# Kernel optimization log

Hardware: AMD Instinct MI355X
Metric: run time of the kernel (lower is better)

## Reference

```python
import jax, jax.numpy as jnp
import numpy as np

S, B, H, K, P = 512, 64, 8, 12, 9        # seq_len, input_bits, num_heads, bits_per_neuron, position bits
L = 2 * B + P                            # head input bits = 137
T = 2 ** K                               # RAM table entries per neuron = 4096
THRESH = H // 2                          # majority-vote threshold


def setup_inputs() -> dict:
    key = jax.random.key(0)
    k1, k2, k3 = jax.random.split(key, 3)
    tokens = jax.random.randint(k1, (S, B), 0, 2, dtype=jnp.int32)           # bit tokens
    conn = jax.random.randint(k2, (H, B, K), 0, L, dtype=jnp.int32)          # random neuron connections
    ram = jnp.round(jax.random.uniform(k3, (H, B, T), dtype=jnp.float32))    # binary RAM contents
    return {"tokens": tokens, "conn": conn, "ram": ram}


def _partial_addr(bits, idx, mask, w):
    # bits: [M, nbits] int; idx/mask: [H,B,K]; w: [K]. Returns [H,B,M] partial RAM address.
    g = bits[:, idx]                                           # [M,H,B,K]
    contrib = jnp.sum(g * (mask.astype(jnp.int32) * w), axis=-1)  # [M,H,B]
    return jnp.moveaxis(contrib, 0, -1)                        # [H,B,M]


def reference(tokens, conn, ram):
    w = (2 ** jnp.arange(K)).astype(jnp.int32)                 # bit weight per connection slot
    # Each connection reads from concat(query_bits[B], key_bits[B], rel_pos_bits[P]).
    is_q = conn < B
    is_k = (conn >= B) & (conn < 2 * B)
    is_r = conn >= 2 * B
    qi = jnp.where(is_q, conn, 0)
    ki = jnp.where(is_k, conn - B, 0)
    ri = jnp.where(is_r, conn - 2 * B, 0)
    d = jnp.arange(S)
    relbits = ((d[:, None] >> jnp.arange(P)) & 1).astype(jnp.int32)  # [S,P] binary rel distance
    # RAM address decomposes additively over the three bit sources.
    Aq = _partial_addr(tokens, qi, is_q, w)                    # [H,B,S] query part (per i)
    Ak = _partial_addr(tokens, ki, is_k, w)                    # [H,B,S] key part (per j)
    Ar = _partial_addr(relbits, ri, is_r, w)                   # [H,B,S] rel-dist part (per i-j)
    dij = jnp.maximum(d[:, None] - d[None, :], 0)              # [S,S] causal rel distance
    addr = Aq[:, :, :, None] + Ak[:, :, None, :] + Ar[:, :, dij]  # [H,B,S,S]
    val = jnp.take_along_axis(ram, addr.reshape(H, B, S * S), axis=2).reshape(H, B, S, S)
    mask = jnp.tril(jnp.ones((S, S), dtype=val.dtype))         # causal: only j <= i contribute
    parity = jnp.mod(jnp.sum(val * mask, axis=-1), 2.0)        # XOR accumulation over keys -> [H,B,S]
    votes = jnp.sum(parity, axis=0)                            # [B,S] ones-count across heads
    out = (votes > THRESH).astype(jnp.float32).T               # [S,B] bit-majority vote
    return out
```

## Files before the change

### kernel.cpp

```cpp
#include <hip/hip_runtime.h>
#include <stdint.h>

#define WS_TABLE 0
#define WS_AK    65536
#define WS_AQ    196608
#define WS_PAR   327680

__global__ __launch_bounds__(256) void softram_pack_kernel(
    const int* __restrict__ tokens,
    const int* __restrict__ conn,
    const float* __restrict__ ram,
    uint32_t* __restrict__ ws)
{
    const int tid = threadIdx.x, lane = tid & 63, w = tid >> 6;
    if (blockIdx.x < 512) {
        const int hb = blockIdx.x;
        const float* ramp = ram + (size_t)hb * 4096;
        uint32_t* tp = ws + WS_TABLE + hb * 128;
        #pragma unroll
        for (int c = 0; c < 16; ++c) {
            float v = ramp[c * 256 + tid];
            unsigned long long m = __ballot(v > 0.5f);
            if (lane == 0) {
                tp[c * 8 + w * 2]     = (uint32_t)m;
                tp[c * 8 + w * 2 + 1] = (uint32_t)(m >> 32);
            }
        }
    } else {
        const int hb = blockIdx.x - 512;
        const int* cp = conn + hb * 12;
        int ck[12];
        #pragma unroll
        for (int k = 0; k < 12; ++k) ck[k] = cp[k];
        unsigned short* akg = (unsigned short*)(ws + WS_AK) + hb * 512;
        unsigned short* aqg = (unsigned short*)(ws + WS_AQ) + hb * 512;
        #pragma unroll
        for (int rep = 0; rep < 2; ++rep) {
            int s = tid + rep * 256;
            int aq = 0, ak = 0;
            #pragma unroll
            for (int k = 0; k < 12; ++k) {
                int c = ck[k];
                if (c < 64)       aq |= tokens[s * 64 + c] << k;
                else if (c < 128) ak |= tokens[s * 64 + (c - 64)] << k;
            }
            aqg[s] = (unsigned short)aq;
            akg[s] = (unsigned short)ak;
        }
    }
}

__global__ __launch_bounds__(256) void softram_parity_kernel(
    const int* __restrict__ conn, uint32_t* __restrict__ ws)
{
    __shared__ uint32_t tbl[128];
    __shared__ unsigned short AkL[512];
    __shared__ unsigned short ArL[512];
    __shared__ unsigned long long parbuf[2][4];

    const int tid  = threadIdx.x;
    const int lane = tid & 63;
    const int w    = tid >> 6;
    const int hb   = blockIdx.x >> 2;
    const int q    = blockIdx.x & 3;

    if (tid < 128) tbl[tid] = ws[WS_TABLE + hb * 128 + tid];
    ((uint32_t*)AkL)[tid] = ws[WS_AK + hb * 256 + tid];

    const int* cp = conn + hb * 12;
    int ck[12];
    #pragma unroll
    for (int k = 0; k < 12; ++k) ck[k] = cp[k];
    int p0 = 0, m0 = 0, p1 = 0, m1 = 0, nr = 0;
    #pragma unroll
    for (int k = 0; k < 12; ++k) {
        int cv = ck[k];
        if (cv >= 128) {
            if (nr == 0)      { p0 = cv - 128; m0 = 1 << k; }
            else if (nr == 1) { p1 = cv - 128; m1 = 1 << k; }
            ++nr;
        }
    }

    #pragma unroll
    for (int rep = 0; rep < 2; ++rep) {
        int s = tid + rep * 256;
        int ar = 0;
        #pragma unroll
        for (int k = 0; k < 12; ++k) {
            int cv = ck[k];
            if (cv >= 128) ar += ((s >> (cv - 128)) & 1) << k;
        }
        ArL[s] = (unsigned short)ar;
    }
    __syncthreads();

    const unsigned short* aqg = (const unsigned short*)(ws + WS_AQ) + hb * 512;
    const int chunks[2] = { q, 7 - q };
    uint32_t accs[2];

    for (int ci = 0; ci < 2; ++ci) {
        const int c  = chunks[ci];
        const int aq = (int)aqg[c * 64 + lane];
        uint32_t acc = 0;
        if (nr <= 2) {
            for (int sb = w; sb < c; sb += 4) {
                int akv = (int)AkL[sb * 64 + lane];
                int dbase = (c - sb) * 64 + lane;
                #pragma unroll
                for (int jj = 0; jj < 64; ++jj) {
                    int sak = __builtin_amdgcn_readlane(akv, jj);
                    int d = dbase - jj;
                    int addr = aq + sak + ((d >> p0) & 1) * m0
                                        + ((d >> p1) & 1) * m1;
                    acc ^= tbl[addr >> 5] >> (addr & 31);
                }
            }
            if (w == (c & 3)) {
                int akv = (int)AkL[c * 64 + lane];
                #pragma unroll
                for (int jj = 0; jj < 64; ++jj) {
                    int sak = __builtin_amdgcn_readlane(akv, jj);
                    int d = lane - jj;
                    int addr = aq + sak + ((d >> p0) & 1) * m0
                                        + ((d >> p1) & 1) * m1;
                    uint32_t keep = ~(uint32_t)(d >> 31);
                    acc ^= (tbl[addr >> 5] >> (addr & 31)) & keep;
                }
            }
        } else {
            for (int sb = w; sb <= c; sb += 4) {
                int akv = (int)AkL[sb * 64 + lane];
                int dbase = (c - sb) * 64 + lane;
                #pragma unroll 8
                for (int jj = 0; jj < 64; ++jj) {
                    int sak = __builtin_amdgcn_readlane(akv, jj);
                    int d = dbase - jj;
                    int dm = d < 0 ? 0 : d;
                    int addr = aq + sak + (int)ArL[dm];
                    uint32_t keep = ~(uint32_t)(d >> 31);
                    acc ^= (tbl[addr >> 5] >> (addr & 31)) & keep;
                }
            }
        }
        accs[ci] = acc & 1u;
    }

    #pragma unroll
    for (int ci = 0; ci < 2; ++ci) {
        unsigned long long m = __ballot(accs[ci] != 0);
        if (lane == 0) parbuf[ci][w] = m;
    }
    __syncthreads();

    if (tid == 0) {
        uint32_t* wp = ws + WS_PAR;
        #pragma unroll
        for (int ci = 0; ci < 2; ++ci) {
            int c = chunks[ci];
            unsigned long long m = parbuf[ci][0] ^ parbuf[ci][1]
                                 ^ parbuf[ci][2] ^ parbuf[ci][3];
            wp[(hb * 8 + c) * 2]     = (uint32_t)m;
            wp[(hb * 8 + c) * 2 + 1] = (uint32_t)(m >> 32);
        }
    }
}

__global__ __launch_bounds__(256) void softram_vote_kernel(
    const uint32_t* __restrict__ ws, float* __restrict__ out)
{
    int t = blockIdx.x * 256 + threadIdx.x;
    int b = t & 63;
    int i = t >> 6;
    const uint32_t* wp = ws + WS_PAR;
    int sum = 0;
    #pragma unroll
    for (int h = 0; h < 8; ++h) {
        int hb = h * 64 + b;
        uint32_t wv = wp[(hb * 8 + (i >> 6)) * 2 + ((i >> 5) & 1)];
        sum += (wv >> (i & 31)) & 1u;
    }
    out[t] = (sum > 4) ? 1.0f : 0.0f;
}

extern "C" void kernel_launch(void* const* d_in, const int* in_sizes, int n_in,
                              void* d_out, int out_size, void* d_ws, size_t ws_size,
                              hipStream_t stream) {
    const int*   tokens = (const int*)d_in[0];
    const int*   conn   = (const int*)d_in[1];
    const float* ram    = (const float*)d_in[2];
    float*       out    = (float*)d_out;
    uint32_t*    ws     = (uint32_t*)d_ws;

    softram_pack_kernel<<<1024, 256, 0, stream>>>(tokens, conn, ram, ws);
    softram_parity_kernel<<<2048, 256, 0, stream>>>(conn, ws);
    softram_vote_kernel<<<128, 256, 0, stream>>>(ws, out);
}
```

Baseline: 119.1 us.

## Fuse RAM table and address packing into parity kernel with byte-per-entry table

Drops the separate pack stage for RAM bits and partial addresses. The parity kernel now loads the float RAM directly and stores it as one byte per entry in shared memory, which removes the shift and mask on every lookup. Query, key and relative-position partial addresses are built per block from bit-packed token rows produced by a small new token kernel. The inner loop is specialised by a template on the number of relative-position connections. In exchange, each of the four blocks per head-bit re-reads the 16 KB RAM row and recomputes the addresses, and the shared table grows from 512 B to 4 KB.

```diff
diff --git a/kernel.cpp b/kernel.cpp
--- a/kernel.cpp
+++ b/kernel.cpp
@@ -1,61 +1,82 @@
 #include <hip/hip_runtime.h>
 #include <stdint.h>
 
-#define WS_TABLE 0
-#define WS_AK    65536
-#define WS_AQ    196608
-#define WS_PAR   327680
-
-__global__ __launch_bounds__(256) void softram_pack_kernel(
+#define WS_TOK 0
+#define WS_PAR 1024
+
+__global__ __launch_bounds__(256) void softram_tok_kernel(
     const int* __restrict__ tokens,
+    uint32_t* __restrict__ ws)
+{
+    const int tid = threadIdx.x, lane = tid & 63, w = tid >> 6;
+    unsigned long long* tokp = (unsigned long long*)(ws + WS_TOK);
+    const int c0 = blockIdx.x * 4;
+    #pragma unroll
+    for (int g = 0; g < 4; ++g) {
+        int c = c0 + g;
+        int v = tokens[c * 256 + tid];
+        unsigned long long m = __ballot(v != 0);
+        if (lane == 0) tokp[c * 4 + w] = m;
+    }
+}
+
+template<int NR>
+__device__ __forceinline__ uint32_t do_chunk(
+    int c, int w, int lane, int aq, int p0, int m0, int p1, int m1,
+    const unsigned short* AkL, const unsigned short* ArL, const uint8_t* tbl)
+{
+    uint32_t acc = 0;
+    for (int sb = w; sb < c; sb += 4) {
+        int akv = (int)AkL[sb * 64 + lane];
+        int dbase = (c - sb) * 64 + lane;
+        #pragma unroll
+        for (int jj = 0; jj < 64; ++jj) {
+            int sak = __builtin_amdgcn_readlane(akv, jj);
+            int addr = aq + sak;
+            if (NR == 1) {
+                int d = dbase - jj;
+                addr += (0 - ((d >> p0) & 1)) & m0;
+            } else if (NR == 2) {
+                int d = dbase - jj;
+                addr += (0 - ((d >> p0) & 1)) & m0;
+                addr += (0 - ((d >> p1) & 1)) & m1;
+            } else if (NR >= 3) {
+                int d = dbase - jj;
+                addr += (int)ArL[d];
+            }
+            acc ^= tbl[addr];
+        }
+    }
+    if (w == (c & 3)) {
+        int akv = (int)AkL[c * 64 + lane];
+        #pragma unroll
+        for (int jj = 0; jj < 64; ++jj) {
+            int sak = __builtin_amdgcn_readlane(akv, jj);
+            int d = lane - jj;
+            int dm = d & ~(d >> 31);
+            int addr = aq + sak;
+            if (NR == 1) {
+                addr += (0 - ((dm >> p0) & 1)) & m0;
+            } else if (NR == 2) {
+                addr += (0 - ((dm >> p0) & 1)) & m0;
+                addr += (0 - ((dm >> p1) & 1)) & m1;
+            } else if (NR >= 3) {
+                addr += (int)ArL[dm];
+            }
+            uint32_t keep = (uint32_t)(~(d >> 31));
+            acc ^= tbl[addr] & keep;
+        }
+    }
+    return acc;
+}
+
+__global__ __launch_bounds__(256) void softram_parity_kernel(
     const int* __restrict__ conn,
     const float* __restrict__ ram,
     uint32_t* __restrict__ ws)
 {
-    const int tid = threadIdx.x, lane = tid & 63, w = tid >> 6;
-    if (blockIdx.x < 512) {
-        const int hb = blockIdx.x;
-        const float* ramp = ram + (size_t)hb * 4096;
-        uint32_t* tp = ws + WS_TABLE + hb * 128;
-        #pragma unroll
-        for (int c = 0; c < 16; ++c) {
-            float v = ramp[c * 256 + tid];
-            unsigned long long m = __ballot(v > 0.5f);
-            if (lane == 0) {
-                tp[c * 8 + w * 2]     = (uint32_t)m;
-                tp[c * 8 + w * 2 + 1] = (uint32_t)(m >> 32);
-            }
-        }
-    } else {
-        const int hb = blockIdx.x - 512;
-        const int* cp = conn + hb * 12;
-        int ck[12];
-        #pragma unroll
-        for (int k = 0; k < 12; ++k) ck[k] = cp[k];
-        unsigned short* akg = (unsigned short*)(ws + WS_AK) + hb * 512;
-        unsigned short* aqg = (unsigned short*)(ws + WS_AQ) + hb * 512;
-        #pragma unroll
-        for (int rep = 0; rep < 2; ++rep) {
-            int s = tid + rep * 256;
-            int aq = 0, ak = 0;
-            #pragma unroll
-            for (int k = 0; k < 12; ++k) {
-                int c = ck[k];
-                if (c < 64)       aq |= tokens[s * 64 + c] << k;
-                else if (c < 128) ak |= tokens[s * 64 + (c - 64)] << k;
-            }
-            aqg[s] = (unsigned short)aq;
-            akg[s] = (unsigned short)ak;
-        }
-    }
-}
-
-__global__ __launch_bounds__(256) void softram_parity_kernel(
-    const int* __restrict__ conn, uint32_t* __restrict__ ws)
-{
-    __shared__ uint32_t tbl[128];
-    __shared__ unsigned short AkL[512];
-    __shared__ unsigned short ArL[512];
+    __shared__ uint8_t tbl[4096];
+    __shared__ unsigned short AqL[512], AkL[512], ArL[512];
     __shared__ unsigned long long parbuf[2][4];
 
     const int tid  = threadIdx.x;
@@ -64,8 +85,19 @@
     const int hb   = blockIdx.x >> 2;
     const int q    = blockIdx.x & 3;
 
-    if (tid < 128) tbl[tid] = ws[WS_TABLE + hb * 128 + tid];
-    ((uint32_t*)AkL)[tid] = ws[WS_AK + hb * 256 + tid];
+    {
+        const float4* rp4 = (const float4*)(ram + (size_t)hb * 4096);
+        uint32_t* tbl32 = (uint32_t*)tbl;
+        #pragma unroll
+        for (int c = 0; c < 4; ++c) {
+            float4 f = rp4[c * 256 + tid];
+            uint32_t b = (f.x > 0.5f ? 1u : 0u)
+                       | (f.y > 0.5f ? 0x100u : 0u)
+                       | (f.z > 0.5f ? 0x10000u : 0u)
+                       | (f.w > 0.5f ? 0x1000000u : 0u);
+            tbl32[c * 256 + tid] = b;
+        }
+    }
 
     const int* cp = conn + hb * 12;
     int ck[12];
@@ -82,68 +114,38 @@
         }
     }
 
+    const unsigned long long* tokp = (const unsigned long long*)(ws + WS_TOK);
     #pragma unroll
     for (int rep = 0; rep < 2; ++rep) {
         int s = tid + rep * 256;
-        int ar = 0;
+        unsigned long long row = tokp[s];
+        int aq = 0, ak = 0, ar = 0;
         #pragma unroll
         for (int k = 0; k < 12; ++k) {
             int cv = ck[k];
-            if (cv >= 128) ar += ((s >> (cv - 128)) & 1) << k;
-        }
+            if (cv < 64)       aq |= (int)((row >> cv) & 1ull) << k;
+            else if (cv < 128) ak |= (int)((row >> (cv - 64)) & 1ull) << k;
+            else               ar += ((s >> (cv - 128)) & 1) << k;
+        }
+        AqL[s] = (unsigned short)aq;
+        AkL[s] = (unsigned short)ak;
         ArL[s] = (unsigned short)ar;
     }
     __syncthreads();
 
-    const unsigned short* aqg = (const unsigned short*)(ws + WS_AQ) + hb * 512;
     const int chunks[2] = { q, 7 - q };
     uint32_t accs[2];
 
+    #pragma unroll 1
     for (int ci = 0; ci < 2; ++ci) {
         const int c  = chunks[ci];
-        const int aq = (int)aqg[c * 64 + lane];
-        uint32_t acc = 0;
-        if (nr <= 2) {
-            for (int sb = w; sb < c; sb += 4) {
-                int akv = (int)AkL[sb * 64 + lane];
-                int dbase = (c - sb) * 64 + lane;
-                #pragma unroll
-                for (int jj = 0; jj < 64; ++jj) {
-                    int sak = __builtin_amdgcn_readlane(akv, jj);
-                    int d = dbase - jj;
-                    int addr = aq + sak + ((d >> p0) & 1) * m0
-                                        + ((d >> p1) & 1) * m1;
-                    acc ^= tbl[addr >> 5] >> (addr & 31);
-                }
-            }
-            if (w == (c & 3)) {
-                int akv = (int)AkL[c * 64 + lane];
-                #pragma unroll
-                for (int jj = 0; jj < 64; ++jj) {
-                    int sak = __builtin_amdgcn_readlane(akv, jj);
-                    int d = lane - jj;
-                    int addr = aq + sak + ((d >> p0) & 1) * m0
-                                        + ((d >> p1) & 1) * m1;
-                    uint32_t keep = ~(uint32_t)(d >> 31);
-                    acc ^= (tbl[addr >> 5] >> (addr & 31)) & keep;
-                }
-            }
-        } else {
-            for (int sb = w; sb <= c; sb += 4) {
-                int akv = (int)AkL[sb * 64 + lane];
-                int dbase = (c - sb) * 64 + lane;
-                #pragma unroll 8
-                for (int jj = 0; jj < 64; ++jj) {
-                    int sak = __builtin_amdgcn_readlane(akv, jj);
-                    int d = dbase - jj;
-                    int dm = d < 0 ? 0 : d;
-                    int addr = aq + sak + (int)ArL[dm];
-                    uint32_t keep = ~(uint32_t)(d >> 31);
-                    acc ^= (tbl[addr >> 5] >> (addr & 31)) & keep;
-                }
-            }
-        }
-        accs[ci] = acc & 1u;
+        const int aq = (int)AqL[c * 64 + lane];
+        uint32_t a;
+        if      (nr == 0) a = do_chunk<0>(c, w, lane, aq, p0, m0, p1, m1, AkL, ArL, tbl);
+        else if (nr == 1) a = do_chunk<1>(c, w, lane, aq, p0, m0, p1, m1, AkL, ArL, tbl);
+        else if (nr == 2) a = do_chunk<2>(c, w, lane, aq, p0, m0, p1, m1, AkL, ArL, tbl);
+        else              a = do_chunk<3>(c, w, lane, aq, p0, m0, p1, m1, AkL, ArL, tbl);
+        accs[ci] = a & 1u;
     }
 
     #pragma unroll
@@ -192,7 +194,7 @@
     float*       out    = (float*)d_out;
     uint32_t*    ws     = (uint32_t*)d_ws;
 
-    softram_pack_kernel<<<1024, 256, 0, stream>>>(tokens, conn, ram, ws);
-    softram_parity_kernel<<<2048, 256, 0, stream>>>(conn, ws);
+    softram_tok_kernel<<<32, 256, 0, stream>>>(tokens, ws);
+    softram_parity_kernel<<<2048, 256, 0, stream>>>(conn, ram, ws);
     softram_vote_kernel<<<128, 256, 0, stream>>>(ws, out);
 }
```

Result: slower. 168.2 us (+41.2%).

## Add prefix-XOR fast path for neurons without relative-position connections

Applied to the files above, without the earlier changes.

Adds a separate kernel for neurons that have no relative-position connections and 3 to 8 key connections. For these, the causal XOR over keys becomes a wave-wide prefix XOR of one-hot key-address masks, followed by a popcount against a per-query-address row of the RAM table. A flag per neuron tells the brute-force parity kernel to skip those neurons, and the pack kernel gains extra blocks that bit-pack token rows. This removes per-key table lookups for a large share of neurons, at the cost of one more launch and a mostly serial single-wave loop per neuron. The token-packing loop also appears to read and write past the intended range.

```diff
diff --git a/kernel.cpp b/kernel.cpp
--- a/kernel.cpp
+++ b/kernel.cpp
@@ -5,6 +5,8 @@
 #define WS_AK    65536
 #define WS_AQ    196608
 #define WS_PAR   327680
+#define WS_TOK   335872
+#define WS_FLAG  336896
 
 __global__ __launch_bounds__(256) void softram_pack_kernel(
     const int* __restrict__ tokens,
@@ -26,7 +28,7 @@
                 tp[c * 8 + w * 2 + 1] = (uint32_t)(m >> 32);
             }
         }
-    } else {
+    } else if (blockIdx.x < 1024) {
         const int hb = blockIdx.x - 512;
         const int* cp = conn + hb * 12;
         int ck[12];
@@ -47,6 +49,115 @@
             aqg[s] = (unsigned short)aq;
             akg[s] = (unsigned short)ak;
         }
+    } else {
+        const int r = blockIdx.x - 1024;
+        unsigned long long* tokp = (unsigned long long*)(ws + WS_TOK);
+        #pragma unroll
+        for (int g = 0; g < 16; ++g) {
+            int c = r * 16 + g;
+            int v = tokens[c * 256 + tid];
+            unsigned long long m = __ballot(v != 0);
+            if (lane == 0) tokp[c * 4 + w] = m;
+        }
+    }
+}
+
+template<int W64>
+__device__ __forceinline__ void fast_rows(
+    int hb, int lane, const int* ck, const unsigned long long* TL,
+    const unsigned long long* tokp, uint32_t* wp)
+{
+    unsigned long long carry[W64];
+    #pragma unroll
+    for (int wd = 0; wd < W64; ++wd) carry[wd] = 0ull;
+
+    for (int g = 0; g < 8; ++g) {
+        int i = g * 64 + lane;
+        unsigned long long row = tokp[i];
+        int aqc = 0, akc = 0, qc = 0, kc = 0;
+        #pragma unroll
+        for (int k = 0; k < 12; ++k) {
+            int cv = ck[k];
+            if (cv < 64)       { aqc |= (int)((row >> cv) & 1ull) << qc; ++qc; }
+            else if (cv < 128) { akc |= (int)((row >> (cv - 64)) & 1ull) << kc; ++kc; }
+        }
+        unsigned long long X[W64];
+        #pragma unroll
+        for (int wd = 0; wd < W64; ++wd)
+            X[wd] = (wd == (akc >> 6)) ? (1ull << (akc & 63)) : 0ull;
+        #pragma unroll
+        for (int off = 1; off < 64; off <<= 1) {
+            #pragma unroll
+            for (int wd = 0; wd < W64; ++wd) {
+                unsigned long long t = __shfl_up(X[wd], off);
+                if (lane >= off) X[wd] ^= t;
+            }
+        }
+        int pc = 0;
+        #pragma unroll
+        for (int wd = 0; wd < W64; ++wd)
+            pc += __popcll(TL[aqc * W64 + wd] & (carry[wd] ^ X[wd]));
+        unsigned long long m = __ballot(pc & 1);
+        if (lane == 0) {
+            wp[(hb * 8 + g) * 2]     = (uint32_t)m;
+            wp[(hb * 8 + g) * 2 + 1] = (uint32_t)(m >> 32);
+        }
+        #pragma unroll
+        for (int wd = 0; wd < W64; ++wd) carry[wd] ^= __shfl(X[wd], 63);
+    }
+}
+
+__global__ __launch_bounds__(256) void softram_fast_kernel(
+    const int* __restrict__ conn, uint32_t* __restrict__ ws)
+{
+    __shared__ uint32_t tblL[128];
+    __shared__ unsigned long long TL[512];
+
+    const int tid = threadIdx.x, lane = tid & 63, w = tid >> 6;
+    const int hb  = blockIdx.x;
+
+    const int* cp = conn + hb * 12;
+    int ck[12];
+    #pragma unroll
+    for (int k = 0; k < 12; ++k) ck[k] = cp[k];
+    int nq = 0, nk = 0, nr = 0;
+    #pragma unroll
+    for (int k = 0; k < 12; ++k) {
+        int cv = ck[k];
+        if (cv < 64) ++nq; else if (cv < 128) ++nk; else ++nr;
+    }
+    const bool fast = (nr == 0) && (nk >= 3) && (nk <= 8);
+    if (tid == 0) ws[WS_FLAG + hb] = fast ? 0u : 1u;
+    if (!fast) return;
+
+    if (tid < 128) tblL[tid] = ws[WS_TABLE + hb * 128 + tid];
+    __syncthreads();
+
+    const int rsh  = (nk > 6) ? (nk - 6) : 0;
+    const int Wtot = (1 << nq) << rsh;
+    for (int wi = w; wi < Wtot; wi += 4) {
+        int a  = wi >> rsh;
+        int mw = wi & ((1 << rsh) - 1);
+        int m  = (mw << 6) | lane;
+        int spread = 0, qc = 0, kc = 0;
+        #pragma unroll
+        for (int k = 0; k < 12; ++k) {
+            int cv = ck[k];
+            if (cv < 64)       { spread |= ((a >> qc) & 1) << k; ++qc; }
+            else if (cv < 128) { spread |= ((m >> kc) & 1) << k; ++kc; }
+        }
+        int bit = (m < (1 << nk)) ? (int)((tblL[spread >> 5] >> (spread & 31)) & 1u) : 0;
+        unsigned long long bm = __ballot(bit != 0);
+        if (lane == 0) TL[wi] = bm;
+    }
+    __syncthreads();
+
+    if (w == 0) {
+        const unsigned long long* tokp = (const unsigned long long*)(ws + WS_TOK);
+        uint32_t* wp = ws + WS_PAR;
+        if (nk <= 6)      fast_rows<1>(hb, lane, ck, TL, tokp, wp);
+        else if (nk == 7) fast_rows<2>(hb, lane, ck, TL, tokp, wp);
+        else              fast_rows<4>(hb, lane, ck, TL, tokp, wp);
     }
 }
 
@@ -64,6 +175,8 @@
     const int hb   = blockIdx.x >> 2;
     const int q    = blockIdx.x & 3;
 
+    if (ws[WS_FLAG + hb] == 0u) return;
+
     if (tid < 128) tbl[tid] = ws[WS_TABLE + hb * 128 + tid];
     ((uint32_t*)AkL)[tid] = ws[WS_AK + hb * 256 + tid];
 
@@ -71,13 +184,13 @@
     int ck[12];
     #pragma unroll
     for (int k = 0; k < 12; ++k) ck[k] = cp[k];
-    int p0 = 0, m0 = 0, p1 = 0, m1 = 0, nr = 0;
+    int p0 = 15, k0 = 0, p1 = 15, k1 = 0, nr = 0;
     #pragma unroll
     for (int k = 0; k < 12; ++k) {
         int cv = ck[k];
         if (cv >= 128) {
-            if (nr == 0)      { p0 = cv - 128; m0 = 1 << k; }
-            else if (nr == 1) { p1 = cv - 128; m1 = 1 << k; }
+            if (nr == 0)      { p0 = cv - 128; k0 = k; }
+            else if (nr == 1) { p1 = cv - 128; k1 = k; }
             ++nr;
         }
     }
@@ -111,8 +224,8 @@
                 for (int jj = 0; jj < 64; ++jj) {
                     int sak = __builtin_amdgcn_readlane(akv, jj);
                     int d = dbase - jj;
-                    int addr = aq + sak + ((d >> p0) & 1) * m0
-                                        + ((d >> p1) & 1) * m1;
+                    int addr = aq + sak + (((d >> p0) & 1) << k0)
+                                        + (((d >> p1) & 1) << k1);
                     acc ^= tbl[addr >> 5] >> (addr & 31);
                 }
             }
@@ -122,8 +235,9 @@
                 for (int jj = 0; jj < 64; ++jj) {
                     int sak = __builtin_amdgcn_readlane(akv, jj);
                     int d = lane - jj;
-                    int addr = aq + sak + ((d >> p0) & 1) * m0
-                                        + ((d >> p1) & 1) * m1;
+                    int dm = d & ~(d >> 31);
+                    int addr = aq + sak + (((dm >> p0) & 1) << k0)
+                                        + (((dm >> p1) & 1) << k1);
                     uint32_t keep = ~(uint32_t)(d >> 31);
                     acc ^= (tbl[addr >> 5] >> (addr & 31)) & keep;
                 }
@@ -136,7 +250,7 @@
                 for (int jj = 0; jj < 64; ++jj) {
                     int sak = __builtin_amdgcn_readlane(akv, jj);
                     int d = dbase - jj;
-                    int dm = d < 0 ? 0 : d;
+                    int dm = d & ~(d >> 31);
                     int addr = aq + sak + (int)ArL[dm];
                     uint32_t keep = ~(uint32_t)(d >> 31);
                     acc ^= (tbl[addr >> 5] >> (addr & 31)) & keep;
@@ -192,7 +306,8 @@
     float*       out    = (float*)d_out;
     uint32_t*    ws     = (uint32_t*)d_ws;
 
-    softram_pack_kernel<<<1024, 256, 0, stream>>>(tokens, conn, ram, ws);
+    softram_pack_kernel<<<1056, 256, 0, stream>>>(tokens, conn, ram, ws);
+    softram_fast_kernel<<<512, 256, 0, stream>>>(conn, ws);
     softram_parity_kernel<<<2048, 256, 0, stream>>>(conn, ws);
     softram_vote_kernel<<<128, 256, 0, stream>>>(ws, out);
 }
```

Result: slower. 175.2 us (+47.1%).

## Pack tokens into bitmasks and compute query/key addresses per parity block

Applied to the files above, without the earlier changes.

The pack kernel now ballots the tokens into 64-bit row bitmasks instead of computing per-(head,bit) query and key partial addresses. Each parity block rebuilds Aq, Ak and Ar in shared memory from these bitmasks, which removes the 512 gather-heavy pack blocks and the larger workspace traffic. The price is that this address computation is repeated in each of the 4 blocks per head-bit. It also replaces the rel-position multiplies with shifts and the diagonal clamp with a branch-free mask.

```diff
diff --git a/kernel.cpp b/kernel.cpp
--- a/kernel.cpp
+++ b/kernel.cpp
@@ -2,13 +2,11 @@
 #include <stdint.h>
 
 #define WS_TABLE 0
-#define WS_AK    65536
-#define WS_AQ    196608
-#define WS_PAR   327680
+#define WS_TOK   65536
+#define WS_PAR   66560
 
 __global__ __launch_bounds__(256) void softram_pack_kernel(
     const int* __restrict__ tokens,
-    const int* __restrict__ conn,
     const float* __restrict__ ram,
     uint32_t* __restrict__ ws)
 {
@@ -27,35 +25,24 @@
             }
         }
     } else {
-        const int hb = blockIdx.x - 512;
-        const int* cp = conn + hb * 12;
-        int ck[12];
+        const int r = blockIdx.x - 512;
+        unsigned long long* tokp = (unsigned long long*)(ws + WS_TOK);
         #pragma unroll
-        for (int k = 0; k < 12; ++k) ck[k] = cp[k];
-        unsigned short* akg = (unsigned short*)(ws + WS_AK) + hb * 512;
-        unsigned short* aqg = (unsigned short*)(ws + WS_AQ) + hb * 512;
-        #pragma unroll
-        for (int rep = 0; rep < 2; ++rep) {
-            int s = tid + rep * 256;
-            int aq = 0, ak = 0;
-            #pragma unroll
-            for (int k = 0; k < 12; ++k) {
-                int c = ck[k];
-                if (c < 64)       aq |= tokens[s * 64 + c] << k;
-                else if (c < 128) ak |= tokens[s * 64 + (c - 64)] << k;
-            }
-            aqg[s] = (unsigned short)aq;
-            akg[s] = (unsigned short)ak;
+        for (int g = 0; g < 4; ++g) {
+            int c = r * 4 + g;
+            int v = tokens[c * 256 + tid];
+            unsigned long long m = __ballot(v != 0);
+            if (lane == 0) tokp[c * 4 + w] = m;
         }
     }
 }
 
 __global__ __launch_bounds__(256) void softram_parity_kernel(
-    const int* __restrict__ conn, uint32_t* __restrict__ ws)
+    const int* __restrict__ conn,
+    uint32_t* __restrict__ ws)
 {
     __shared__ uint32_t tbl[128];
-    __shared__ unsigned short AkL[512];
-    __shared__ unsigned short ArL[512];
+    __shared__ unsigned short AqL[512], AkL[512], ArL[512];
     __shared__ unsigned long long parbuf[2][4];
 
     const int tid  = threadIdx.x;
@@ -65,43 +52,47 @@
     const int q    = blockIdx.x & 3;
 
     if (tid < 128) tbl[tid] = ws[WS_TABLE + hb * 128 + tid];
-    ((uint32_t*)AkL)[tid] = ws[WS_AK + hb * 256 + tid];
 
     const int* cp = conn + hb * 12;
     int ck[12];
     #pragma unroll
     for (int k = 0; k < 12; ++k) ck[k] = cp[k];
-    int p0 = 0, m0 = 0, p1 = 0, m1 = 0, nr = 0;
+    int p0 = 15, k0 = 0, p1 = 15, k1 = 0, nr = 0;
     #pragma unroll
     for (int k = 0; k < 12; ++k) {
         int cv = ck[k];
         if (cv >= 128) {
-            if (nr == 0)      { p0 = cv - 128; m0 = 1 << k; }
-            else if (nr == 1) { p1 = cv - 128; m1 = 1 << k; }
+            if (nr == 0)      { p0 = cv - 128; k0 = k; }
+            else if (nr == 1) { p1 = cv - 128; k1 = k; }
             ++nr;
         }
     }
 
+    const unsigned long long* tokp = (const unsigned long long*)(ws + WS_TOK);
     #pragma unroll
     for (int rep = 0; rep < 2; ++rep) {
         int s = tid + rep * 256;
-        int ar = 0;
+        unsigned long long row = tokp[s];
+        int aq = 0, ak = 0, ar = 0;
         #pragma unroll
         for (int k = 0; k < 12; ++k) {
             int cv = ck[k];
-            if (cv >= 128) ar += ((s >> (cv - 128)) & 1) << k;
+            if (cv < 64)       aq |= (int)((row >> cv) & 1ull) << k;
+            else if (cv < 128) ak |= (int)((row >> (cv - 64)) & 1ull) << k;
+            else               ar += ((s >> (cv - 128)) & 1) << k;
         }
+        AqL[s] = (unsigned short)aq;
+        AkL[s] = (unsigned short)ak;
         ArL[s] = (unsigned short)ar;
     }
     __syncthreads();
 
-    const unsigned short* aqg = (const unsigned short*)(ws + WS_AQ) + hb * 512;
     const int chunks[2] = { q, 7 - q };
     uint32_t accs[2];
 
     for (int ci = 0; ci < 2; ++ci) {
         const int c  = chunks[ci];
-        const int aq = (int)aqg[c * 64 + lane];
+        const int aq = (int)AqL[c * 64 + lane];
         uint32_t acc = 0;
         if (nr <= 2) {
             for (int sb = w; sb < c; sb += 4) {
@@ -111,8 +102,8 @@
                 for (int jj = 0; jj < 64; ++jj) {
                     int sak = __builtin_amdgcn_readlane(akv, jj);
                     int d = dbase - jj;
-                    int addr = aq + sak + ((d >> p0) & 1) * m0
-                                        + ((d >> p1) & 1) * m1;
+                    int addr = aq + sak + (((d >> p0) & 1) << k0)
+                                        + (((d >> p1) & 1) << k1);
                     acc ^= tbl[addr >> 5] >> (addr & 31);
                 }
             }
@@ -122,8 +113,9 @@
                 for (int jj = 0; jj < 64; ++jj) {
                     int sak = __builtin_amdgcn_readlane(akv, jj);
                     int d = lane - jj;
-                    int addr = aq + sak + ((d >> p0) & 1) * m0
-                                        + ((d >> p1) & 1) * m1;
+                    int dm = d & ~(d >> 31);
+                    int addr = aq + sak + (((dm >> p0) & 1) << k0)
+                                        + (((dm >> p1) & 1) << k1);
                     uint32_t keep = ~(uint32_t)(d >> 31);
                     acc ^= (tbl[addr >> 5] >> (addr & 31)) & keep;
                 }
@@ -136,7 +128,7 @@
                 for (int jj = 0; jj < 64; ++jj) {
                     int sak = __builtin_amdgcn_readlane(akv, jj);
                     int d = dbase - jj;
-                    int dm = d < 0 ? 0 : d;
+                    int dm = d & ~(d >> 31);
                     int addr = aq + sak + (int)ArL[dm];
                     uint32_t keep = ~(uint32_t)(d >> 31);
                     acc ^= (tbl[addr >> 5] >> (addr & 31)) & keep;
@@ -192,7 +184,7 @@
     float*       out    = (float*)d_out;
     uint32_t*    ws     = (uint32_t*)d_ws;
 
-    softram_pack_kernel<<<1024, 256, 0, stream>>>(tokens, conn, ram, ws);
+    softram_pack_kernel<<<544, 256, 0, stream>>>(tokens, ram, ws);
     softram_parity_kernel<<<2048, 256, 0, stream>>>(conn, ws);
     softram_vote_kernel<<<128, 256, 0, stream>>>(ws, out);
 }
```

New measurement: 109.7 us. 1.09x faster.
